# Kernel tuning notes

Measured on AMD Instinct MI355X. Metric: run time of the kernel, lower is better.

## Reference

```python
import jax, jax.numpy as jnp
import numpy as np

N_NODES = 100000
N_EDGES = 3200000
IN_FEAT = 512
HIDDEN = 16
N_CLASSES = 40


def gcn_conv(x, W, b, row, col, n):
    """PyG-style GCNConv: linear transform, add self-loops, symmetric deg^-1/2
    normalization, gather-scatter aggregation, bias."""
    self_idx = jnp.arange(n, dtype=row.dtype)
    row_sl = jnp.concatenate([row, self_idx])  # [E + N]
    col_sl = jnp.concatenate([col, self_idx])
    deg = jax.ops.segment_sum(jnp.ones_like(row_sl, dtype=x.dtype), row_sl, num_segments=n)
    dinv = jnp.where(deg > 0, jax.lax.rsqrt(deg), 0.0)
    norm = dinv[row_sl] * dinv[col_sl]  # [E + N]
    h = x @ W  # [n, out] -- transform first (cheap since out dim is small)
    msg = h[col_sl] * norm[:, None]  # gather + scale
    out = jax.ops.segment_sum(msg, row_sl, num_segments=n)  # scatter-add
    return out + b


def setup_inputs() -> dict:
    key = jax.random.key(0)
    k1, k2, k3, k4, k5 = jax.random.split(key, 5)
    x = jax.random.normal(k1, (N_NODES, IN_FEAT), dtype=jnp.float32)
    edge_index = jax.random.randint(k2, (2, N_EDGES), 0, N_NODES, dtype=jnp.int64)
    # Glorot-style init for linear weights
    W1 = jax.random.normal(k3, (IN_FEAT, HIDDEN), dtype=jnp.float32) / np.sqrt(IN_FEAT)
    b1 = jnp.zeros((HIDDEN,), dtype=jnp.float32)
    W2 = jax.random.normal(k4, (HIDDEN, N_CLASSES), dtype=jnp.float32) / np.sqrt(HIDDEN)
    b2 = jnp.zeros((N_CLASSES,), dtype=jnp.float32)
    return {"x": x, "edge_index": edge_index, "W1": W1, "b1": b1, "W2": W2, "b2": b2}


def reference(x, edge_index, W1, b1, W2, b2):
    row, col = edge_index[0], edge_index[1]
    n = x.shape[0]
    h = jax.nn.relu(gcn_conv(x, W1, b1, row, col, n))
    # dropout is identity at inference (training=False)
    out = gcn_conv(h, W2, b2, row, col, n)
    return jax.nn.log_softmax(out, axis=1)
```

## Files before the change

kernel.cpp:

```cpp
#include <hip/hip_runtime.h>

#define NFEAT 512
#define HID 16
#define NCLS 40
#define BROWS 256
#define BCAP 16384

typedef unsigned int uint32;
typedef float f4 __attribute__((ext_vector_type(4)));

__device__ __forceinline__ uint32 f2bf(float f) {
    uint32 u = __float_as_uint(f);
    return (u + 0x7FFFu + ((u >> 16) & 1u)) >> 16;
}
__device__ __forceinline__ float bf2f(uint32 h) {
    return __uint_as_float(h << 16);
}

__global__ void k_zero(int* __restrict__ p, int m) {
    int i = blockIdx.x * blockDim.x + threadIdx.x;
    if (i < m) p[i] = 0;
}

__global__ __launch_bounds__(256) void k_pairs(const int* __restrict__ row,
                                               const int* __restrict__ col,
                                               int* __restrict__ bcur,
                                               uint32* __restrict__ pairs, int E, int nb) {
    __shared__ int lhist[512];
    __shared__ int lbase[512];
    int chunk = (E + gridDim.x - 1) / gridDim.x;
    int s = blockIdx.x * chunk;
    int e = min(s + chunk, E);
    for (int b = threadIdx.x; b < nb; b += 256) lhist[b] = 0;
    __syncthreads();
    for (int i = s + threadIdx.x; i < e; i += 256)
        atomicAdd(&lhist[row[i] >> 8], 1);
    __syncthreads();
    for (int b = threadIdx.x; b < nb; b += 256) {
        int h = lhist[b];
        lbase[b] = h ? atomicAdd(&bcur[b], h) : 0;
        lhist[b] = 0;
    }
    __syncthreads();
    for (int i = s + threadIdx.x; i < e; i += 256) {
        int r = row[i], c = col[i];
        int b = r >> 8;
        int off = lbase[b] + atomicAdd(&lhist[b], 1);
        if (off < BCAP)
            pairs[(size_t)b * BCAP + off] = ((uint32)(r & 255) << 17) | (uint32)c;
    }
}

__global__ __launch_bounds__(256) void k_csr(const int* __restrict__ bcur,
                                             const uint32* __restrict__ pairs,
                                             int* __restrict__ csr,
                                             int* __restrict__ start, int* __restrict__ end,
                                             float* __restrict__ dinv, int n) {
    __shared__ int lhist[256];
    __shared__ int sm[256];
    __shared__ int lcur[256];
    int b = blockIdx.x;
    int base = b * BROWS;
    int i = base + threadIdx.x;
    int bo = b * BCAP;
    int cnt = min(bcur[b], BCAP);
    int e2 = bo + cnt;

    lhist[threadIdx.x] = 0;
    __syncthreads();
    for (int p = bo + (int)threadIdx.x; p < e2; p += 256)
        atomicAdd(&lhist[pairs[p] >> 17], 1);
    __syncthreads();
    int c = lhist[threadIdx.x];
    if (i < n) dinv[i] = rsqrtf((float)c + 1.0f);
    sm[threadIdx.x] = c;
    __syncthreads();
    for (int off = 1; off < 256; off <<= 1) {
        int t = (threadIdx.x >= off) ? sm[threadIdx.x - off] : 0;
        __syncthreads();
        sm[threadIdx.x] += t;
        __syncthreads();
    }
    int excl = sm[threadIdx.x] - c;
    lcur[threadIdx.x] = excl;
    if (i < n) {
        start[i] = bo + excl;
        end[i]   = bo + excl + c;
    }
    __syncthreads();
    for (int p = bo + (int)threadIdx.x; p < e2; p += 256) {
        uint32 pk = pairs[p];
        int off = atomicAdd(&lcur[pk >> 17], 1);
        csr[bo + off] = (int)(pk & 0x1FFFFu);
    }
}

__global__ __launch_bounds__(256, 4) void k_gemm1(const float* __restrict__ x,
                                                  const float* __restrict__ W,
                                                  const float* __restrict__ dinv,
                                                  uint32* __restrict__ g1, int n) {
    __shared__ float Wl[8704];
    const int tid = threadIdx.x;
    const int ks = tid & 7;
    const int g  = tid >> 3;

#pragma unroll
    for (int i = 0; i < 8; i++) {
        int fidx = tid + i * 256;
        int k = fidx >> 2, j4 = fidx & 3;
        float4 v = reinterpret_cast<const float4*>(W)[fidx];
        *reinterpret_cast<float4*>(&Wl[k * 16 + (k >> 2) * 4 + j4 * 4]) = v;
    }
    __syncthreads();

    const int rbase = blockIdx.x * 64 + g * 2;
    const int r0 = min(rbase, n - 1);
    const int r1 = min(rbase + 1, n - 1);
    const f4* xq0 = reinterpret_cast<const f4*>(x + (size_t)r0 * NFEAT);
    const f4* xq1 = reinterpret_cast<const f4*>(x + (size_t)r1 * NFEAT);

    float acc[2][16];
#pragma unroll
    for (int rr = 0; rr < 2; rr++)
#pragma unroll
        for (int j = 0; j < 16; j++) acc[rr][j] = 0.f;

    f4 xv[2], xn[2];
    xv[0] = __builtin_nontemporal_load(&xq0[ks]);
    xv[1] = __builtin_nontemporal_load(&xq1[ks]);

    for (int c = 0; c < 16; c++) {
        if (c < 15) {
            xn[0] = __builtin_nontemporal_load(&xq0[(c + 1) * 8 + ks]);
            xn[1] = __builtin_nontemporal_load(&xq1[(c + 1) * 8 + ks]);
        }
#pragma unroll
        for (int m = 0; m < 4; m++) {
            int k = c * 32 + ks * 4 + m;
            const float* wrow = &Wl[k * 16 + (k >> 2) * 4];
            float4 wv[4];
#pragma unroll
            for (int j4 = 0; j4 < 4; j4++)
                wv[j4] = *reinterpret_cast<const float4*>(wrow + j4 * 4);
#pragma unroll
            for (int rr = 0; rr < 2; rr++) {
                float xs = xv[rr][m];
#pragma unroll
                for (int j4 = 0; j4 < 4; j4++) {
                    acc[rr][j4 * 4 + 0] = fmaf(xs, wv[j4].x, acc[rr][j4 * 4 + 0]);
                    acc[rr][j4 * 4 + 1] = fmaf(xs, wv[j4].y, acc[rr][j4 * 4 + 1]);
                    acc[rr][j4 * 4 + 2] = fmaf(xs, wv[j4].z, acc[rr][j4 * 4 + 2]);
                    acc[rr][j4 * 4 + 3] = fmaf(xs, wv[j4].w, acc[rr][j4 * 4 + 3]);
                }
            }
        }
        xv[0] = xn[0];
        xv[1] = xn[1];
    }

#pragma unroll
    for (int off = 1; off < 8; off <<= 1)
#pragma unroll
        for (int rr = 0; rr < 2; rr++)
#pragma unroll
            for (int j = 0; j < 16; j++)
                acc[rr][j] += __shfl_xor(acc[rr][j], off, 8);

    if (ks == 0) {
#pragma unroll
        for (int rr = 0; rr < 2; rr++) {
            int r = rbase + rr;
            if (r < n) {
                float dr = dinv[r];
                uint32 us[8];
#pragma unroll
                for (int q = 0; q < 8; q++) {
                    uint32 lo = f2bf(dr * acc[rr][q * 2]);
                    uint32 hi = f2bf(dr * acc[rr][q * 2 + 1]);
                    us[q] = lo | (hi << 16);
                }
                uint4* o = reinterpret_cast<uint4*>(g1 + (size_t)r * 8);
                o[0] = make_uint4(us[0], us[1], us[2], us[3]);
                o[1] = make_uint4(us[4], us[5], us[6], us[7]);
            }
        }
    }
}

__global__ __launch_bounds__(256) void k_agg1(const uint32* __restrict__ g1,
                                              const int* __restrict__ start,
                                              const int* __restrict__ end,
                                              const int* __restrict__ csr,
                                              const float* __restrict__ dinv,
                                              const float* __restrict__ b1,
                                              uint32* __restrict__ g2, int n) {
    int g = threadIdx.x >> 3;
    int l = threadIdx.x & 7;
    int r = blockIdx.x * 32 + g;
    if (r >= n) return;
    int s = start[r], e = end[r];
    float a0 = 0.f, a1 = 0.f;
    int p = s;
    for (; p + 8 <= e; p += 8) {
        int c[8];
#pragma unroll
        for (int u = 0; u < 8; u++) c[u] = csr[p + u];
        uint32 hv[8];
#pragma unroll
        for (int u = 0; u < 8; u++) hv[u] = g1[c[u] * 8 + l];
#pragma unroll
        for (int u = 0; u < 8; u++) {
            a0 += bf2f(hv[u] & 0xFFFFu);
            a1 += bf2f(hv[u] >> 16);
        }
    }
    for (; p < e; p++) {
        uint32 h = g1[csr[p] * 8 + l];
        a0 += bf2f(h & 0xFFFFu);
        a1 += bf2f(h >> 16);
    }
    uint32 hs = g1[r * 8 + l];
    float dr = dinv[r];
    float z0 = fmaf(dr, a0 + bf2f(hs & 0xFFFFu), b1[2 * l]);
    float z1 = fmaf(dr, a1 + bf2f(hs >> 16), b1[2 * l + 1]);
    g2[r * 8 + l] = f2bf(dr * fmaxf(z0, 0.f)) | (f2bf(dr * fmaxf(z1, 0.f)) << 16);
}

__global__ __launch_bounds__(256) void k_agg2(const uint32* __restrict__ g2,
                                              const int* __restrict__ start,
                                              const int* __restrict__ end,
                                              const int* __restrict__ csr,
                                              const float* __restrict__ dinv,
                                              const float* __restrict__ W2,
                                              const float* __restrict__ b2,
                                              float* __restrict__ out, int n) {
    __shared__ float vsm[32][17];
    int g = threadIdx.x >> 3;
    int l = threadIdx.x & 7;
    int r = blockIdx.x * 32 + g;
    float a0 = 0.f, a1 = 0.f;
    if (r < n) {
        int s = start[r], e = end[r];
        int p = s;
        for (; p + 8 <= e; p += 8) {
            int c[8];
#pragma unroll
            for (int u = 0; u < 8; u++) c[u] = csr[p + u];
            uint32 hv[8];
#pragma unroll
            for (int u = 0; u < 8; u++) hv[u] = g2[c[u] * 8 + l];
#pragma unroll
            for (int u = 0; u < 8; u++) {
                a0 += bf2f(hv[u] & 0xFFFFu);
                a1 += bf2f(hv[u] >> 16);
            }
        }
        for (; p < e; p++) {
            uint32 h = g2[csr[p] * 8 + l];
            a0 += bf2f(h & 0xFFFFu);
            a1 += bf2f(h >> 16);
        }
        uint32 hs = g2[r * 8 + l];
        float dr = dinv[r];
        a0 = dr * (a0 + bf2f(hs & 0xFFFFu));
        a1 = dr * (a1 + bf2f(hs >> 16));
    }
    vsm[g][2 * l] = a0;
    vsm[g][2 * l + 1] = a1;
    __syncthreads();
    if (r >= n) return;

    float vloc[16];
#pragma unroll
    for (int k = 0; k < 16; k++) vloc[k] = vsm[g][k];

    float z[5];
#pragma unroll
    for (int i = 0; i < 5; i++) z[i] = b2[l + 8 * i];
#pragma unroll
    for (int k = 0; k < 16; k++) {
        float vk = vloc[k];
        const float* wk = W2 + k * NCLS;
#pragma unroll
        for (int i = 0; i < 5; i++) z[i] = fmaf(vk, wk[l + 8 * i], z[i]);
    }
    float m = z[0];
#pragma unroll
    for (int i = 1; i < 5; i++) m = fmaxf(m, z[i]);
#pragma unroll
    for (int off = 1; off < 8; off <<= 1) m = fmaxf(m, __shfl_xor(m, off, 8));
    float ssum = 0.f;
#pragma unroll
    for (int i = 0; i < 5; i++) ssum += __expf(z[i] - m);
#pragma unroll
    for (int off = 1; off < 8; off <<= 1) ssum += __shfl_xor(ssum, off, 8);
    float ls = m + logf(ssum);
    float* o = out + (size_t)r * NCLS;
#pragma unroll
    for (int i = 0; i < 5; i++) o[l + 8 * i] = z[i] - ls;
}


extern "C" void kernel_launch(void* const* d_in, const int* in_sizes, int n_in,
                              void* d_out, int out_size, void* d_ws, size_t ws_size,
                              hipStream_t stream) {
    const float* x  = (const float*)d_in[0];
    const int*   ei = (const int*)d_in[1];
    const float* W1 = (const float*)d_in[2];
    const float* b1 = (const float*)d_in[3];
    const float* W2 = (const float*)d_in[4];
    const float* b2 = (const float*)d_in[5];

    const int n = in_sizes[0] / NFEAT;
    const int E = in_sizes[1] / 2;
    const int* row = ei;
    const int* col = ei + E;
    const int nb = (n + BROWS - 1) / BROWS;

    char* w = (char*)d_ws;
    auto alloc = [&](size_t bytes) {
        void* p = (void*)w;
        w += (bytes + 255) & ~(size_t)255;
        return p;
    };
    int*    start = (int*)alloc((size_t)n * 4);
    int*    end   = (int*)alloc((size_t)n * 4);
    int*    bcur  = (int*)alloc(2048);
    float*  dinv  = (float*)alloc((size_t)n * 4);
    int*    csr   = (int*)alloc((size_t)nb * BCAP * 4);
    uint32* pairs = (uint32*)alloc((size_t)nb * BCAP * 4);
    uint32* g1    = (uint32*)alloc((size_t)n * HID * 2);
    uint32* g2    = (uint32*)alloc((size_t)n * HID * 2);

    k_zero<<<1, 512, 0, stream>>>(bcur, nb);
    k_pairs<<<512, 256, 0, stream>>>(row, col, bcur, pairs, E, nb);
    k_csr<<<nb, 256, 0, stream>>>(bcur, pairs, csr, start, end, dinv, n);

    k_gemm1<<<(n + 63) / 64, 256, 0, stream>>>(x, W1, dinv, g1, n);
    k_agg1<<<(n + 31) / 32, 256, 0, stream>>>(g1, start, end, csr, dinv, b1, g2, n);
    k_agg2<<<(n + 31) / 32, 256, 0, stream>>>(g2, start, end, csr, dinv, W2, b2,
                                              (float*)d_out, n);
}
```

Before: 188.3 us.

## Fuse edge bucketing with first GEMM and move dinv scaling into aggregation

The edge-pair bucketing kernel and the x@W1 GEMM now run as one launch, with the first 256 blocks doing bucketing and the rest doing the GEMM. This lets the GEMM overlap with CSR construction and no longer depends on dinv. The source-node dinv scaling moves into agg1 as an extra gather of dinv[c] per edge. Bucketing now uses 256 blocks instead of 512, and agg1 does more random loads per edge in exchange.

```diff
diff --git a/kernel.cpp b/kernel.cpp
--- a/kernel.cpp
+++ b/kernel.cpp
@@ -5,6 +5,7 @@
 #define NCLS 40
 #define BROWS 256
 #define BCAP 16384
+#define PAIRS_BLOCKS 256
 
 typedef unsigned int uint32;
 typedef float f4 __attribute__((ext_vector_type(4)));
@@ -22,32 +23,127 @@
     if (i < m) p[i] = 0;
 }
 
-__global__ __launch_bounds__(256) void k_pairs(const int* __restrict__ row,
-                                               const int* __restrict__ col,
-                                               int* __restrict__ bcur,
-                                               uint32* __restrict__ pairs, int E, int nb) {
-    __shared__ int lhist[512];
-    __shared__ int lbase[512];
-    int chunk = (E + gridDim.x - 1) / gridDim.x;
-    int s = blockIdx.x * chunk;
-    int e = min(s + chunk, E);
-    for (int b = threadIdx.x; b < nb; b += 256) lhist[b] = 0;
-    __syncthreads();
-    for (int i = s + threadIdx.x; i < e; i += 256)
-        atomicAdd(&lhist[row[i] >> 8], 1);
-    __syncthreads();
-    for (int b = threadIdx.x; b < nb; b += 256) {
-        int h = lhist[b];
-        lbase[b] = h ? atomicAdd(&bcur[b], h) : 0;
-        lhist[b] = 0;
-    }
-    __syncthreads();
-    for (int i = s + threadIdx.x; i < e; i += 256) {
-        int r = row[i], c = col[i];
-        int b = r >> 8;
-        int off = lbase[b] + atomicAdd(&lhist[b], 1);
-        if (off < BCAP)
-            pairs[(size_t)b * BCAP + off] = ((uint32)(r & 255) << 17) | (uint32)c;
+__global__ __launch_bounds__(256, 4) void k_fused1(const float* __restrict__ x,
+                                                   const float* __restrict__ W,
+                                                   uint32* __restrict__ h1, int n,
+                                                   const int* __restrict__ row,
+                                                   const int* __restrict__ col,
+                                                   int* __restrict__ bcur,
+                                                   uint32* __restrict__ pairs,
+                                                   int E, int nb) {
+    __shared__ float smem[8704];
+    const int tid = threadIdx.x;
+
+    if (blockIdx.x < PAIRS_BLOCKS) {
+        int* lhist = (int*)smem;
+        int* lbase = (int*)smem + 512;
+        int chunk = (E + PAIRS_BLOCKS - 1) / PAIRS_BLOCKS;
+        int s = blockIdx.x * chunk;
+        int e = min(s + chunk, E);
+        for (int b = tid; b < nb; b += 256) lhist[b] = 0;
+        __syncthreads();
+        for (int i = s + tid; i < e; i += 256)
+            atomicAdd(&lhist[row[i] >> 8], 1);
+        __syncthreads();
+        for (int b = tid; b < nb; b += 256) {
+            int h = lhist[b];
+            lbase[b] = h ? atomicAdd(&bcur[b], h) : 0;
+            lhist[b] = 0;
+        }
+        __syncthreads();
+        for (int i = s + tid; i < e; i += 256) {
+            int r = row[i], c = col[i];
+            int b = r >> 8;
+            int off = lbase[b] + atomicAdd(&lhist[b], 1);
+            if (off < BCAP)
+                pairs[(size_t)b * BCAP + off] = ((uint32)(r & 255) << 17) | (uint32)c;
+        }
+        return;
+    }
+
+    float* Wl = smem;
+    const int ks = tid & 7;
+    const int g  = tid >> 3;
+
+#pragma unroll
+    for (int i = 0; i < 8; i++) {
+        int fidx = tid + i * 256;
+        int k = fidx >> 2, j4 = fidx & 3;
+        float4 v = reinterpret_cast<const float4*>(W)[fidx];
+        *reinterpret_cast<float4*>(&Wl[k * 16 + (k >> 2) * 4 + j4 * 4]) = v;
+    }
+    __syncthreads();
+
+    const int rbase = (blockIdx.x - PAIRS_BLOCKS) * 64 + g * 2;
+    const int r0 = min(rbase, n - 1);
+    const int r1 = min(rbase + 1, n - 1);
+    const f4* xq0 = reinterpret_cast<const f4*>(x + (size_t)r0 * NFEAT);
+    const f4* xq1 = reinterpret_cast<const f4*>(x + (size_t)r1 * NFEAT);
+
+    float acc[2][16];
+#pragma unroll
+    for (int rr = 0; rr < 2; rr++)
+#pragma unroll
+        for (int j = 0; j < 16; j++) acc[rr][j] = 0.f;
+
+    f4 xv[2], xn[2];
+    xv[0] = __builtin_nontemporal_load(&xq0[ks]);
+    xv[1] = __builtin_nontemporal_load(&xq1[ks]);
+
+    for (int c = 0; c < 16; c++) {
+        if (c < 15) {
+            xn[0] = __builtin_nontemporal_load(&xq0[(c + 1) * 8 + ks]);
+            xn[1] = __builtin_nontemporal_load(&xq1[(c + 1) * 8 + ks]);
+        }
+#pragma unroll
+        for (int m = 0; m < 4; m++) {
+            int k = c * 32 + ks * 4 + m;
+            const float* wrow = &Wl[k * 16 + (k >> 2) * 4];
+            float4 wv[4];
+#pragma unroll
+            for (int j4 = 0; j4 < 4; j4++)
+                wv[j4] = *reinterpret_cast<const float4*>(wrow + j4 * 4);
+#pragma unroll
+            for (int rr = 0; rr < 2; rr++) {
+                float xs = xv[rr][m];
+#pragma unroll
+                for (int j4 = 0; j4 < 4; j4++) {
+                    acc[rr][j4 * 4 + 0] = fmaf(xs, wv[j4].x, acc[rr][j4 * 4 + 0]);
+                    acc[rr][j4 * 4 + 1] = fmaf(xs, wv[j4].y, acc[rr][j4 * 4 + 1]);
+                    acc[rr][j4 * 4 + 2] = fmaf(xs, wv[j4].z, acc[rr][j4 * 4 + 2]);
+                    acc[rr][j4 * 4 + 3] = fmaf(xs, wv[j4].w, acc[rr][j4 * 4 + 3]);
+                }
+            }
+        }
+        xv[0] = xn[0];
+        xv[1] = xn[1];
+    }
+
+#pragma unroll
+    for (int off = 1; off < 8; off <<= 1)
+#pragma unroll
+        for (int rr = 0; rr < 2; rr++)
+#pragma unroll
+            for (int j = 0; j < 16; j++)
+                acc[rr][j] += __shfl_xor(acc[rr][j], off, 8);
+
+    if (ks == 0) {
+#pragma unroll
+        for (int rr = 0; rr < 2; rr++) {
+            int r = rbase + rr;
+            if (r < n) {
+                uint32 us[8];
+#pragma unroll
+                for (int q = 0; q < 8; q++) {
+                    uint32 lo = f2bf(acc[rr][q * 2]);
+                    uint32 hi = f2bf(acc[rr][q * 2 + 1]);
+                    us[q] = lo | (hi << 16);
+                }
+                uint4* o = reinterpret_cast<uint4*>(h1 + (size_t)r * 8);
+                o[0] = make_uint4(us[0], us[1], us[2], us[3]);
+                o[1] = make_uint4(us[4], us[5], us[6], us[7]);
+            }
+        }
     }
 }
 
@@ -95,99 +191,7 @@
     }
 }
 
-__global__ __launch_bounds__(256, 4) void k_gemm1(const float* __restrict__ x,
-                                                  const float* __restrict__ W,
-                                                  const float* __restrict__ dinv,
-                                                  uint32* __restrict__ g1, int n) {
-    __shared__ float Wl[8704];
-    const int tid = threadIdx.x;
-    const int ks = tid & 7;
-    const int g  = tid >> 3;
-
-#pragma unroll
-    for (int i = 0; i < 8; i++) {
-        int fidx = tid + i * 256;
-        int k = fidx >> 2, j4 = fidx & 3;
-        float4 v = reinterpret_cast<const float4*>(W)[fidx];
-        *reinterpret_cast<float4*>(&Wl[k * 16 + (k >> 2) * 4 + j4 * 4]) = v;
-    }
-    __syncthreads();
-
-    const int rbase = blockIdx.x * 64 + g * 2;
-    const int r0 = min(rbase, n - 1);
-    const int r1 = min(rbase + 1, n - 1);
-    const f4* xq0 = reinterpret_cast<const f4*>(x + (size_t)r0 * NFEAT);
-    const f4* xq1 = reinterpret_cast<const f4*>(x + (size_t)r1 * NFEAT);
-
-    float acc[2][16];
-#pragma unroll
-    for (int rr = 0; rr < 2; rr++)
-#pragma unroll
-        for (int j = 0; j < 16; j++) acc[rr][j] = 0.f;
-
-    f4 xv[2], xn[2];
-    xv[0] = __builtin_nontemporal_load(&xq0[ks]);
-    xv[1] = __builtin_nontemporal_load(&xq1[ks]);
-
-    for (int c = 0; c < 16; c++) {
-        if (c < 15) {
-            xn[0] = __builtin_nontemporal_load(&xq0[(c + 1) * 8 + ks]);
-            xn[1] = __builtin_nontemporal_load(&xq1[(c + 1) * 8 + ks]);
-        }
-#pragma unroll
-        for (int m = 0; m < 4; m++) {
-            int k = c * 32 + ks * 4 + m;
-            const float* wrow = &Wl[k * 16 + (k >> 2) * 4];
-            float4 wv[4];
-#pragma unroll
-            for (int j4 = 0; j4 < 4; j4++)
-                wv[j4] = *reinterpret_cast<const float4*>(wrow + j4 * 4);
-#pragma unroll
-            for (int rr = 0; rr < 2; rr++) {
-                float xs = xv[rr][m];
-#pragma unroll
-                for (int j4 = 0; j4 < 4; j4++) {
-                    acc[rr][j4 * 4 + 0] = fmaf(xs, wv[j4].x, acc[rr][j4 * 4 + 0]);
-                    acc[rr][j4 * 4 + 1] = fmaf(xs, wv[j4].y, acc[rr][j4 * 4 + 1]);
-                    acc[rr][j4 * 4 + 2] = fmaf(xs, wv[j4].z, acc[rr][j4 * 4 + 2]);
-                    acc[rr][j4 * 4 + 3] = fmaf(xs, wv[j4].w, acc[rr][j4 * 4 + 3]);
-                }
-            }
-        }
-        xv[0] = xn[0];
-        xv[1] = xn[1];
-    }
-
-#pragma unroll
-    for (int off = 1; off < 8; off <<= 1)
-#pragma unroll
-        for (int rr = 0; rr < 2; rr++)
-#pragma unroll
-            for (int j = 0; j < 16; j++)
-                acc[rr][j] += __shfl_xor(acc[rr][j], off, 8);
-
-    if (ks == 0) {
-#pragma unroll
-        for (int rr = 0; rr < 2; rr++) {
-            int r = rbase + rr;
-            if (r < n) {
-                float dr = dinv[r];
-                uint32 us[8];
-#pragma unroll
-                for (int q = 0; q < 8; q++) {
-                    uint32 lo = f2bf(dr * acc[rr][q * 2]);
-                    uint32 hi = f2bf(dr * acc[rr][q * 2 + 1]);
-                    us[q] = lo | (hi << 16);
-                }
-                uint4* o = reinterpret_cast<uint4*>(g1 + (size_t)r * 8);
-                o[0] = make_uint4(us[0], us[1], us[2], us[3]);
-                o[1] = make_uint4(us[4], us[5], us[6], us[7]);
-            }
-        }
-    }
-}
-
-__global__ __launch_bounds__(256) void k_agg1(const uint32* __restrict__ g1,
+__global__ __launch_bounds__(256) void k_agg1(const uint32* __restrict__ h1,
                                               const int* __restrict__ start,
                                               const int* __restrict__ end,
                                               const int* __restrict__ csr,
@@ -206,23 +210,28 @@
 #pragma unroll
         for (int u = 0; u < 8; u++) c[u] = csr[p + u];
         uint32 hv[8];
-#pragma unroll
-        for (int u = 0; u < 8; u++) hv[u] = g1[c[u] * 8 + l];
+        float dv[8];
+#pragma unroll
+        for (int u = 0; u < 8; u++) hv[u] = h1[c[u] * 8 + l];
+#pragma unroll
+        for (int u = 0; u < 8; u++) dv[u] = dinv[c[u]];
 #pragma unroll
         for (int u = 0; u < 8; u++) {
-            a0 += bf2f(hv[u] & 0xFFFFu);
-            a1 += bf2f(hv[u] >> 16);
+            a0 = fmaf(dv[u], bf2f(hv[u] & 0xFFFFu), a0);
+            a1 = fmaf(dv[u], bf2f(hv[u] >> 16), a1);
         }
     }
     for (; p < e; p++) {
-        uint32 h = g1[csr[p] * 8 + l];
-        a0 += bf2f(h & 0xFFFFu);
-        a1 += bf2f(h >> 16);
-    }
-    uint32 hs = g1[r * 8 + l];
+        int c = csr[p];
+        uint32 h = h1[c * 8 + l];
+        float dv = dinv[c];
+        a0 = fmaf(dv, bf2f(h & 0xFFFFu), a0);
+        a1 = fmaf(dv, bf2f(h >> 16), a1);
+    }
+    uint32 hs = h1[r * 8 + l];
     float dr = dinv[r];
-    float z0 = fmaf(dr, a0 + bf2f(hs & 0xFFFFu), b1[2 * l]);
-    float z1 = fmaf(dr, a1 + bf2f(hs >> 16), b1[2 * l + 1]);
+    float z0 = fmaf(dr, fmaf(dr, bf2f(hs & 0xFFFFu), a0), b1[2 * l]);
+    float z1 = fmaf(dr, fmaf(dr, bf2f(hs >> 16), a1), b1[2 * l + 1]);
     g2[r * 8 + l] = f2bf(dr * fmaxf(z0, 0.f)) | (f2bf(dr * fmaxf(z1, 0.f)) << 16);
 }
 
@@ -329,15 +338,14 @@
     float*  dinv  = (float*)alloc((size_t)n * 4);
     int*    csr   = (int*)alloc((size_t)nb * BCAP * 4);
     uint32* pairs = (uint32*)alloc((size_t)nb * BCAP * 4);
-    uint32* g1    = (uint32*)alloc((size_t)n * HID * 2);
+    uint32* h1    = (uint32*)alloc((size_t)n * HID * 2);
     uint32* g2    = (uint32*)alloc((size_t)n * HID * 2);
 
     k_zero<<<1, 512, 0, stream>>>(bcur, nb);
-    k_pairs<<<512, 256, 0, stream>>>(row, col, bcur, pairs, E, nb);
+    k_fused1<<<PAIRS_BLOCKS + (n + 63) / 64, 256, 0, stream>>>(
+        x, W1, h1, n, row, col, bcur, pairs, E, nb);
     k_csr<<<nb, 256, 0, stream>>>(bcur, pairs, csr, start, end, dinv, n);
-
-    k_gemm1<<<(n + 63) / 64, 256, 0, stream>>>(x, W1, dinv, g1, n);
-    k_agg1<<<(n + 31) / 32, 256, 0, stream>>>(g1, start, end, csr, dinv, b1, g2, n);
+    k_agg1<<<(n + 31) / 32, 256, 0, stream>>>(h1, start, end, csr, dinv, b1, g2, n);
     k_agg2<<<(n + 31) / 32, 256, 0, stream>>>(g2, start, end, csr, dinv, W2, b2,
                                               (float*)d_out, n);
 }
```

Result: slower. 192.7 us (+2.3%).

## Split CSR build into degree pass and fuse CSR fill with GEMM1 launch

Applied to the files above, without the earlier changes.

Splits the CSR build into two parts. A small kernel now computes per-row degree counts and dinv. A combined kernel then runs the scan and CSR fill in its first nb blocks, while the remaining blocks run the x·W1 GEMM. The aim is to overlap the latency-bound CSR scatter with the bandwidth-bound GEMM in a single launch. The cost is one extra pass over the pairs buffer and an extra count array.

```diff
diff --git a/kernel.cpp b/kernel.cpp
--- a/kernel.cpp
+++ b/kernel.cpp
@@ -51,56 +51,76 @@
     }
 }
 
-__global__ __launch_bounds__(256) void k_csr(const int* __restrict__ bcur,
+__global__ __launch_bounds__(256) void k_deg(const int* __restrict__ bcur,
                                              const uint32* __restrict__ pairs,
-                                             int* __restrict__ csr,
-                                             int* __restrict__ start, int* __restrict__ end,
+                                             int* __restrict__ cnt,
                                              float* __restrict__ dinv, int n) {
-    __shared__ int lhist[256];
-    __shared__ int sm[256];
-    __shared__ int lcur[256];
+    __shared__ int lh[BROWS];
     int b = blockIdx.x;
-    int base = b * BROWS;
-    int i = base + threadIdx.x;
     int bo = b * BCAP;
-    int cnt = min(bcur[b], BCAP);
-    int e2 = bo + cnt;
-
-    lhist[threadIdx.x] = 0;
-    __syncthreads();
-    for (int p = bo + (int)threadIdx.x; p < e2; p += 256)
-        atomicAdd(&lhist[pairs[p] >> 17], 1);
-    __syncthreads();
-    int c = lhist[threadIdx.x];
-    if (i < n) dinv[i] = rsqrtf((float)c + 1.0f);
-    sm[threadIdx.x] = c;
-    __syncthreads();
-    for (int off = 1; off < 256; off <<= 1) {
-        int t = (threadIdx.x >= off) ? sm[threadIdx.x - off] : 0;
-        __syncthreads();
-        sm[threadIdx.x] += t;
-        __syncthreads();
-    }
-    int excl = sm[threadIdx.x] - c;
-    lcur[threadIdx.x] = excl;
+    int c2 = min(bcur[b], BCAP);
+    lh[threadIdx.x] = 0;
+    __syncthreads();
+    for (int p = bo + (int)threadIdx.x; p < bo + c2; p += 256)
+        atomicAdd(&lh[pairs[p] >> 17], 1);
+    __syncthreads();
+    int i = b * BROWS + threadIdx.x;
     if (i < n) {
-        start[i] = bo + excl;
-        end[i]   = bo + excl + c;
-    }
-    __syncthreads();
-    for (int p = bo + (int)threadIdx.x; p < e2; p += 256) {
-        uint32 pk = pairs[p];
-        int off = atomicAdd(&lcur[pk >> 17], 1);
-        csr[bo + off] = (int)(pk & 0x1FFFFu);
-    }
-}
-
-__global__ __launch_bounds__(256, 4) void k_gemm1(const float* __restrict__ x,
+        int c = lh[threadIdx.x];
+        cnt[i] = c;
+        dinv[i] = rsqrtf((float)c + 1.0f);
+    }
+}
+
+__global__ __launch_bounds__(256, 4) void k_fused(const int* __restrict__ bcur,
+                                                  const uint32* __restrict__ pairs,
+                                                  const int* __restrict__ cnt,
+                                                  int* __restrict__ csr,
+                                                  int* __restrict__ start,
+                                                  int* __restrict__ end,
+                                                  const float* __restrict__ x,
                                                   const float* __restrict__ W,
                                                   const float* __restrict__ dinv,
-                                                  uint32* __restrict__ g1, int n) {
-    __shared__ float Wl[8704];
+                                                  uint32* __restrict__ g1,
+                                                  int n, int nbCsr) {
+    __shared__ float smem[8704];
     const int tid = threadIdx.x;
+
+    if (blockIdx.x < (uint32)nbCsr) {
+        int* sm   = (int*)smem;
+        int* lcur = (int*)smem + 256;
+        int b = blockIdx.x;
+        int base = b * BROWS;
+        int i = base + tid;
+        int bo = b * BCAP;
+        int cntb = min(bcur[b], BCAP);
+        int e2 = bo + cntb;
+
+        int c = (i < n) ? cnt[i] : 0;
+        sm[tid] = c;
+        __syncthreads();
+        for (int off = 1; off < 256; off <<= 1) {
+            int t = (tid >= off) ? sm[tid - off] : 0;
+            __syncthreads();
+            sm[tid] += t;
+            __syncthreads();
+        }
+        int excl = sm[tid] - c;
+        lcur[tid] = excl;
+        if (i < n) {
+            start[i] = bo + excl;
+            end[i]   = bo + excl + c;
+        }
+        __syncthreads();
+        for (int p = bo + tid; p < e2; p += 256) {
+            uint32 pk = pairs[p];
+            int off = atomicAdd(&lcur[pk >> 17], 1);
+            csr[bo + off] = (int)(pk & 0x1FFFFu);
+        }
+        return;
+    }
+
+    float* Wl = smem;
     const int ks = tid & 7;
     const int g  = tid >> 3;
 
@@ -113,7 +133,7 @@
     }
     __syncthreads();
 
-    const int rbase = blockIdx.x * 64 + g * 2;
+    const int rbase = (blockIdx.x - nbCsr) * 64 + g * 2;
     const int r0 = min(rbase, n - 1);
     const int r1 = min(rbase + 1, n - 1);
     const f4* xq0 = reinterpret_cast<const f4*>(x + (size_t)r0 * NFEAT);
@@ -325,6 +345,7 @@
     };
     int*    start = (int*)alloc((size_t)n * 4);
     int*    end   = (int*)alloc((size_t)n * 4);
+    int*    cnt   = (int*)alloc((size_t)n * 4);
     int*    bcur  = (int*)alloc(2048);
     float*  dinv  = (float*)alloc((size_t)n * 4);
     int*    csr   = (int*)alloc((size_t)nb * BCAP * 4);
@@ -334,9 +355,9 @@
 
     k_zero<<<1, 512, 0, stream>>>(bcur, nb);
     k_pairs<<<512, 256, 0, stream>>>(row, col, bcur, pairs, E, nb);
-    k_csr<<<nb, 256, 0, stream>>>(bcur, pairs, csr, start, end, dinv, n);
-
-    k_gemm1<<<(n + 63) / 64, 256, 0, stream>>>(x, W1, dinv, g1, n);
+    k_deg<<<nb, 256, 0, stream>>>(bcur, pairs, cnt, dinv, n);
+    k_fused<<<nb + (n + 63) / 64, 256, 0, stream>>>(bcur, pairs, cnt, csr, start, end,
+                                                    x, W1, dinv, g1, n, nb);
     k_agg1<<<(n + 31) / 32, 256, 0, stream>>>(g1, start, end, csr, dinv, b1, g2, n);
     k_agg2<<<(n + 31) / 32, 256, 0, stream>>>(g2, start, end, csr, dinv, W2, b2,
                                               (float*)d_out, n);
```

Measured after the change: 186.3 us. Within noise of the previous version (-1.0%).
